# Performance work log

Hardware: AMD Instinct MI355X
Metric: run time of the kernel (lower is better)

The kernel has to match this reference:

```python
import jax, jax.numpy as jnp
import numpy as np
from math import sqrt

B, N, M, HID, NH = 16, 512, 1024, 512, 8
HS = HID // NH  # 64


def layer_norm(x, g, b, eps=1e-5):
    mu = jnp.mean(x, axis=-1, keepdims=True)
    var = jnp.var(x, axis=-1, keepdims=True)
    return (x - mu) * jax.lax.rsqrt(var + eps) * g + b


def apply_moverz(x, s, c):
    # x: [B, L, NH, HS]; s, c: [B, L, 1, HS//2]
    x0, x1 = x[..., 0::2], x[..., 1::2]
    return jnp.concatenate([x0 * c - x1 * s, x1 * c + x0 * s], axis=-1)


def attention(q, k, v, mask):
    # q: [B,Nq,NH,HS], k/v: [B,Nk,NH,HS], mask broadcastable to [B,NH,Nq,Nk]
    attn = jnp.einsum('bnhd,bmhd->bhnm', q, k) / sqrt(HS)
    attn = jnp.where(mask, -jnp.inf, attn)
    attn = jax.nn.softmax(attn, axis=-1)
    x = jnp.einsum('bhnm,bmhd->bnhd', attn, v)
    return x.reshape(x.shape[0], x.shape[1], HID)


def setup_inputs() -> dict:
    key = jax.random.key(0)
    ks = jax.random.split(key, 24)
    inp = {}
    inp['tgt'] = jax.random.normal(ks[0], (B, N, HID), dtype=jnp.float32)
    inp['mem'] = jax.random.normal(ks[1], (B, M, HID), dtype=jnp.float32)
    th_p = jax.random.uniform(ks[2], (B, N, 1, HS // 2), dtype=jnp.float32) * (2 * np.pi)
    th_k = jax.random.uniform(ks[3], (B, M, 1, HS // 2), dtype=jnp.float32) * (2 * np.pi)
    inp['pep_mass_sin'] = jnp.sin(th_p)
    inp['pep_mass_cos'] = jnp.cos(th_p)
    inp['peaks_moverz_sin'] = jnp.sin(th_k)
    inp['peaks_moverz_cos'] = jnp.cos(th_k)
    # causal self-attn mask (True = masked)
    inp['tgt_mask'] = jnp.triu(jnp.ones((N, N), dtype=bool), k=1)[None, None]
    # pad last 64 memory positions
    pad = jnp.arange(M) >= (M - 64)
    inp['mem_key_padding_mask'] = jnp.broadcast_to(pad[None, None, None, :], (B, 1, 1, M))
    s = 0.02
    w = lambda i, shape: jax.random.normal(ks[i], shape, dtype=jnp.float32) * s
    # MaskedMultiHeadAttn params
    inp['mmha_w'] = w(4, (3 * HID, HID)); inp['mmha_b'] = jnp.zeros((3 * HID,), jnp.float32)
    inp['mmha_ow'] = w(5, (HID, HID)); inp['mmha_ob'] = jnp.zeros((HID,), jnp.float32)
    inp['mmha_g'] = jnp.ones((HID,), jnp.float32); inp['mmha_beta'] = jnp.zeros((HID,), jnp.float32)
    # MultiHeadAttn (cross) params
    inp['mha_qw'] = w(6, (HID, HID)); inp['mha_qb'] = jnp.zeros((HID,), jnp.float32)
    inp['mha_kvw'] = w(7, (2 * HID, HID)); inp['mha_kvb'] = jnp.zeros((2 * HID,), jnp.float32)
    inp['mha_ow'] = w(8, (HID, HID)); inp['mha_ob'] = jnp.zeros((HID,), jnp.float32)
    inp['mha_g'] = jnp.ones((HID,), jnp.float32); inp['mha_beta'] = jnp.zeros((HID,), jnp.float32)
    # FFN params (no bias)
    inp['ffn_w1'] = w(9, (4 * HID, HID))
    inp['ffn_w2'] = w(10, (HID, 4 * HID))
    inp['ffn_g'] = jnp.ones((HID,), jnp.float32); inp['ffn_beta'] = jnp.zeros((HID,), jnp.float32)
    return inp


def reference(tgt, mem, pep_mass_sin, pep_mass_cos, peaks_moverz_sin, peaks_moverz_cos,
              tgt_mask, mem_key_padding_mask,
              mmha_w, mmha_b, mmha_ow, mmha_ob, mmha_g, mmha_beta,
              mha_qw, mha_qb, mha_kvw, mha_kvb, mha_ow, mha_ob, mha_g, mha_beta,
              ffn_w1, ffn_w2, ffn_g, ffn_beta):
    # --- masked self-attention ---
    qkv = (tgt @ mmha_w.T + mmha_b).reshape(B, N, NH, 3 * HS)
    q, k, v = jnp.split(qkv, 3, axis=-1)
    x = attention(q, k, v, tgt_mask)
    tgt = layer_norm(x @ mmha_ow.T + mmha_ob + tgt, mmha_g, mmha_beta)
    # --- cross-attention with moverz distance bias ---
    q = (tgt @ mha_qw.T + mha_qb).reshape(B, N, NH, HS)
    q = apply_moverz(q, pep_mass_sin, pep_mass_cos)
    kv = (mem @ mha_kvw.T + mha_kvb).reshape(B, M, NH, 2 * HS)
    k, v = jnp.split(kv, 2, axis=-1)
    k = apply_moverz(k, peaks_moverz_sin, peaks_moverz_cos)
    x = attention(q, k, v, mem_key_padding_mask)
    tgt = layer_norm(x @ mha_ow.T + mha_ob + tgt, mha_g, mha_beta)
    # --- FFN ---
    h = jax.nn.relu(tgt @ ffn_w1.T) @ ffn_w2.T
    tgt = layer_norm(tgt + h, ffn_g, ffn_beta)
    return tgt
```

## Files before the change

### kernel.cpp

```cpp
#include <hip/hip_runtime.h>
#include <hip/hip_bf16.h>

#define BB 16
#define NN 512
#define MM 1024
#define HIDD 512
#define NHH 8

typedef unsigned short ushort_t;
typedef __attribute__((ext_vector_type(8))) short short8;
typedef __attribute__((ext_vector_type(8))) _Float16 half8;
typedef __attribute__((ext_vector_type(4))) _Float16 half4;
typedef __attribute__((ext_vector_type(4))) float f32x4;

__device__ __forceinline__ ushort_t f2bf(float x) {
    unsigned u = __float_as_uint(x);
    u += 0x7fff + ((u >> 16) & 1);
    return (ushort_t)(u >> 16);
}

#define GLD16(g, l) __builtin_amdgcn_global_load_lds(                      \
    (const __attribute__((address_space(1))) void*)(g),                    \
    (__attribute__((address_space(3))) void*)(l), 16, 0, 0)

__device__ __forceinline__ void xcd_swizzle(int& colb, int& rowb) {
    int id = blockIdx.x + blockIdx.y * gridDim.x;
    int C = gridDim.x;
    int xcd = id & 7;
    int slot = id >> 3;
    int rows_per = gridDim.y >> 3;
    colb = slot % C;
    rowb = xcd * rows_per + slot / C;
}

__global__ __launch_bounds__(256)
void gemm_bf(const ushort_t* __restrict__ A, const ushort_t* __restrict__ W,
             const float* __restrict__ bias, float* __restrict__ C,
             ushort_t* __restrict__ Cb, _Float16* __restrict__ Ch,
             int K, int Cout, int relu) {
    __shared__ __align__(16) ushort_t smem[2][8192];
    const int tid = threadIdx.x;
    const int lane = tid & 63;
    const int wid = tid >> 6;
    const int wm = wid >> 1, wn = wid & 1;
    int colb, rowb;
    xcd_swizzle(colb, rowb);
    const long row0 = (long)rowb * 128;
    const long col0 = (long)colb * 128;

    const int sr = lane >> 2;
    const int skq = lane & 3;
    const ushort_t* Ag = A + (row0 + wid * 32 + sr) * (long)K + skq * 8;
    const ushort_t* Wg = W + (col0 + wid * 32 + sr) * (long)K + skq * 8;
    const int sa0 = (wid * 32) * 32, sa1 = (wid * 32 + 16) * 32;

    f32x4 acc[4][4] = {};
    const int lr = lane & 15;
    const int kg = lane >> 4;

    GLD16(Ag, &smem[0][sa0]);
    GLD16(Ag + 16 * (long)K, &smem[0][sa1]);
    GLD16(Wg, &smem[0][4096 + sa0]);
    GLD16(Wg + 16 * (long)K, &smem[0][4096 + sa1]);

    int pb = 0;
    for (int k0 = 0; k0 < K; k0 += 32, pb ^= 1) {
        __syncthreads();
        int kn = k0 + 32;
        if (kn < K) {
            GLD16(Ag + kn, &smem[pb ^ 1][sa0]);
            GLD16(Ag + 16 * (long)K + kn, &smem[pb ^ 1][sa1]);
            GLD16(Wg + kn, &smem[pb ^ 1][4096 + sa0]);
            GLD16(Wg + 16 * (long)K + kn, &smem[pb ^ 1][4096 + sa1]);
        }
        const ushort_t* Ab = smem[pb];
        const ushort_t* Wb = smem[pb] + 4096;
        short8 af[4], bfr[4];
#pragma unroll
        for (int i = 0; i < 4; i++)
            af[i] = *(const short8*)&Ab[(wm * 64 + i * 16 + lr) * 32 + kg * 8];
#pragma unroll
        for (int j = 0; j < 4; j++)
            bfr[j] = *(const short8*)&Wb[(wn * 64 + j * 16 + lr) * 32 + kg * 8];
#pragma unroll
        for (int i = 0; i < 4; i++)
#pragma unroll
            for (int j = 0; j < 4; j++)
                acc[i][j] = __builtin_amdgcn_mfma_f32_16x16x32_bf16(
                    af[i], bfr[j], acc[i][j], 0, 0, 0);
    }

#pragma unroll
    for (int i = 0; i < 4; i++) {
#pragma unroll
        for (int j = 0; j < 4; j++) {
            long row = row0 + wm * 64 + i * 16 + kg * 4;
            long col = col0 + wn * 64 + j * 16 + lr;
            float bv = bias ? bias[col] : 0.f;
#pragma unroll
            for (int r = 0; r < 4; r++) {
                float x = acc[i][j][r] + bv;
                if (relu) x = fmaxf(x, 0.f);
                size_t idx = (row + r) * (size_t)Cout + col;
                if (Ch)      Ch[idx] = (_Float16)x;
                else if (Cb) Cb[idx] = f2bf(x);
                else         C[idx] = x;
            }
        }
    }
}

__global__ __launch_bounds__(256)
void gemm_bf64(const ushort_t* __restrict__ A, const ushort_t* __restrict__ W,
               const float* __restrict__ bias, float* __restrict__ C,
               ushort_t* __restrict__ Cb, _Float16* __restrict__ Ch,
               int K, int Cout, int relu) {
    __shared__ __align__(16) ushort_t smem[2][6144];
    const int tid = threadIdx.x;
    const int lane = tid & 63;
    const int w = tid >> 6;
    int colb, rowb;
    xcd_swizzle(colb, rowb);
    const long row0 = (long)rowb * 128;
    const long col0 = (long)colb * 64;

    const int sr = lane >> 2;
    const int skq = lane & 3;
    const ushort_t* Ag = A + (row0 + w * 32 + sr) * (long)K + skq * 8;
    const ushort_t* Wg = W + (col0 + w * 16 + sr) * (long)K + skq * 8;
    const int sa0 = (w * 32) * 32, sa1 = (w * 32 + 16) * 32;
    const int sw0 = 4096 + (w * 16) * 32;

    f32x4 acc[2][4] = {};
    const int lr = lane & 15;
    const int kg = lane >> 4;

    GLD16(Ag, &smem[0][sa0]);
    GLD16(Ag + 16 * (long)K, &smem[0][sa1]);
    GLD16(Wg, &smem[0][sw0]);

    int pb = 0;
    for (int k0 = 0; k0 < K; k0 += 32, pb ^= 1) {
        __syncthreads();
        int kn = k0 + 32;
        if (kn < K) {
            GLD16(Ag + kn, &smem[pb ^ 1][sa0]);
            GLD16(Ag + 16 * (long)K + kn, &smem[pb ^ 1][sa1]);
            GLD16(Wg + kn, &smem[pb ^ 1][sw0]);
        }
        const ushort_t* Ab = smem[pb];
        const ushort_t* Wb = smem[pb] + 4096;
        short8 af[2], bfr[4];
#pragma unroll
        for (int i = 0; i < 2; i++)
            af[i] = *(const short8*)&Ab[(w * 32 + i * 16 + lr) * 32 + kg * 8];
#pragma unroll
        for (int j = 0; j < 4; j++)
            bfr[j] = *(const short8*)&Wb[(j * 16 + lr) * 32 + kg * 8];
#pragma unroll
        for (int i = 0; i < 2; i++)
#pragma unroll
            for (int j = 0; j < 4; j++)
                acc[i][j] = __builtin_amdgcn_mfma_f32_16x16x32_bf16(
                    af[i], bfr[j], acc[i][j], 0, 0, 0);
    }

#pragma unroll
    for (int i = 0; i < 2; i++) {
#pragma unroll
        for (int j = 0; j < 4; j++) {
            long row = row0 + w * 32 + i * 16 + kg * 4;
            long col = col0 + j * 16 + lr;
            float bv = bias ? bias[col] : 0.f;
#pragma unroll
            for (int r = 0; r < 4; r++) {
                float x = acc[i][j][r] + bv;
                if (relu) x = fmaxf(x, 0.f);
                size_t idx = (row + r) * (size_t)Cout + col;
                if (Ch)      Ch[idx] = (_Float16)x;
                else if (Cb) Cb[idx] = f2bf(x);
                else         C[idx] = x;
            }
        }
    }
}

__global__ __launch_bounds__(256)
void gemm_q_rot(const ushort_t* __restrict__ A, const ushort_t* __restrict__ W,
                const float* __restrict__ bias,
                const float* __restrict__ sn, const float* __restrict__ cs,
                _Float16* __restrict__ Qrot) {
    __shared__ __align__(16) ushort_t smem[2][6144];
    _Float16* Cs = (_Float16*)smem;
    const int K = 512;
    const int tid = threadIdx.x;
    const int lane = tid & 63;
    const int w = tid >> 6;
    int colb, rowb;
    xcd_swizzle(colb, rowb);
    const long row0 = (long)rowb * 128;
    const int h = colb;
    const long col0 = (long)h * 64;

    const int sr = lane >> 2;
    const int skq = lane & 3;
    const ushort_t* Ag = A + (row0 + w * 32 + sr) * (long)K + skq * 8;
    const ushort_t* Wg = W + (col0 + w * 16 + sr) * (long)K + skq * 8;
    const int sa0 = (w * 32) * 32, sa1 = (w * 32 + 16) * 32;
    const int sw0 = 4096 + (w * 16) * 32;

    f32x4 acc[2][4] = {};
    const int lr = lane & 15;
    const int kg = lane >> 4;

    GLD16(Ag, &smem[0][sa0]);
    GLD16(Ag + 16 * (long)K, &smem[0][sa1]);
    GLD16(Wg, &smem[0][sw0]);

    int pb = 0;
    for (int k0 = 0; k0 < K; k0 += 32, pb ^= 1) {
        __syncthreads();
        int kn = k0 + 32;
        if (kn < K) {
            GLD16(Ag + kn, &smem[pb ^ 1][sa0]);
            GLD16(Ag + 16 * (long)K + kn, &smem[pb ^ 1][sa1]);
            GLD16(Wg + kn, &smem[pb ^ 1][sw0]);
        }
        const ushort_t* Ab = smem[pb];
        const ushort_t* Wb = smem[pb] + 4096;
        short8 af[2], bfr[4];
#pragma unroll
        for (int i = 0; i < 2; i++)
            af[i] = *(const short8*)&Ab[(w * 32 + i * 16 + lr) * 32 + kg * 8];
#pragma unroll
        for (int j = 0; j < 4; j++)
            bfr[j] = *(const short8*)&Wb[(j * 16 + lr) * 32 + kg * 8];
#pragma unroll
        for (int i = 0; i < 2; i++)
#pragma unroll
            for (int j = 0; j < 4; j++)
                acc[i][j] = __builtin_amdgcn_mfma_f32_16x16x32_bf16(
                    af[i], bfr[j], acc[i][j], 0, 0, 0);
    }

    __syncthreads();
#pragma unroll
    for (int i = 0; i < 2; i++)
#pragma unroll
        for (int j = 0; j < 4; j++) {
            int row = w * 32 + i * 16 + kg * 4;
            int col = j * 16 + lr;
            float bv = bias[col0 + col];
#pragma unroll
            for (int r = 0; r < 4; r++)
                Cs[(row + r) * 76 + col] = (_Float16)(acc[i][j][r] + bv);
        }
    __syncthreads();
    for (int idx = tid; idx < 4096; idx += 256) {
        int rr = idx >> 5, j = idx & 31;
        size_t srow = (size_t)row0 + rr;
        float x0 = (float)Cs[rr * 76 + 2 * j], x1 = (float)Cs[rr * 76 + 2 * j + 1];
        float s = sn[srow * 32 + j], c = cs[srow * 32 + j];
        Qrot[srow * 512 + h * 64 + j]      = (_Float16)(x0 * c - x1 * s);
        Qrot[srow * 512 + h * 64 + 32 + j] = (_Float16)(x1 * c + x0 * s);
    }
}

__global__ __launch_bounds__(256)
void gemm_kv(const ushort_t* __restrict__ A, const ushort_t* __restrict__ W,
             const float* __restrict__ bias,
             const float* __restrict__ sn, const float* __restrict__ cs,
             _Float16* __restrict__ Krot, _Float16* __restrict__ Vth) {
    __shared__ __align__(16) ushort_t smem[2][8192];
    _Float16* Cs = (_Float16*)smem;
    const int K = 512;
    const int tid = threadIdx.x;
    const int lane = tid & 63;
    const int wid = tid >> 6;
    const int wm = wid >> 1, wn = wid & 1;
    int colb, rowb;
    xcd_swizzle(colb, rowb);
    const long row0 = (long)rowb * 128;
    const int h = colb;
    const long col0 = (long)h * 128;

    const int sr = lane >> 2;
    const int skq = lane & 3;
    const ushort_t* Ag = A + (row0 + wid * 32 + sr) * (long)K + skq * 8;
    const ushort_t* Wg = W + (col0 + wid * 32 + sr) * (long)K + skq * 8;
    const int sa0 = (wid * 32) * 32, sa1 = (wid * 32 + 16) * 32;

    f32x4 acc[4][4] = {};
    const int lr = lane & 15;
    const int kg = lane >> 4;

    GLD16(Ag, &smem[0][sa0]);
    GLD16(Ag + 16 * (long)K, &smem[0][sa1]);
    GLD16(Wg, &smem[0][4096 + sa0]);
    GLD16(Wg + 16 * (long)K, &smem[0][4096 + sa1]);

    int pb = 0;
    for (int k0 = 0; k0 < K; k0 += 32, pb ^= 1) {
        __syncthreads();
        int kn = k0 + 32;
        if (kn < K) {
            GLD16(Ag + kn, &smem[pb ^ 1][sa0]);
            GLD16(Ag + 16 * (long)K + kn, &smem[pb ^ 1][sa1]);
            GLD16(Wg + kn, &smem[pb ^ 1][4096 + sa0]);
            GLD16(Wg + 16 * (long)K + kn, &smem[pb ^ 1][4096 + sa1]);
        }
        const ushort_t* Ab = smem[pb];
        const ushort_t* Wb = smem[pb] + 4096;
        short8 af[4], bfr[4];
#pragma unroll
        for (int i = 0; i < 4; i++)
            af[i] = *(const short8*)&Ab[(wm * 64 + i * 16 + lr) * 32 + kg * 8];
#pragma unroll
        for (int j = 0; j < 4; j++)
            bfr[j] = *(const short8*)&Wb[(wn * 64 + j * 16 + lr) * 32 + kg * 8];
#pragma unroll
        for (int i = 0; i < 4; i++)
#pragma unroll
            for (int j = 0; j < 4; j++)
                acc[i][j] = __builtin_amdgcn_mfma_f32_16x16x32_bf16(
                    af[i], bfr[j], acc[i][j], 0, 0, 0);
    }

    const int b_ = (int)(row0 >> 10);
    const int m0_ = (int)(row0 & 1023);
#pragma unroll
    for (int half = 0; half < 2; half++) {
        __syncthreads();
        if (wn == half) {
#pragma unroll
            for (int i = 0; i < 4; i++)
#pragma unroll
                for (int j = 0; j < 4; j++) {
                    int row = wm * 64 + i * 16 + kg * 4;
                    int col = j * 16 + lr;
                    float bv = bias[col0 + half * 64 + col];
#pragma unroll
                    for (int r = 0; r < 4; r++)
                        Cs[(row + r) * 76 + col] = (_Float16)(acc[i][j][r] + bv);
                }
        }
        __syncthreads();
        if (half == 0) {
            for (int idx = tid; idx < 4096; idx += 256) {
                int rr = idx >> 5, j = idx & 31;
                size_t srow = (size_t)row0 + rr;
                float x0 = (float)Cs[rr * 76 + 2 * j], x1 = (float)Cs[rr * 76 + 2 * j + 1];
                float s = sn[srow * 32 + j], c = cs[srow * 32 + j];
                Krot[srow * 512 + h * 64 + j]      = (_Float16)(x0 * c - x1 * s);
                Krot[srow * 512 + h * 64 + 32 + j] = (_Float16)(x1 * c + x0 * s);
            }
        } else {
            for (int idx = tid; idx < 1024; idx += 256) {
                int d = idx >> 4, c = idx & 15;
                half8 v;
#pragma unroll
                for (int k = 0; k < 8; k++) v[k] = Cs[(c * 8 + k) * 76 + d];
                *(half8*)(Vth + (((size_t)(b_ * NHH + h)) * 64 + d) * MM
                          + m0_ + c * 8) = v;
            }
        }
    }
}

__global__ __launch_bounds__(256)
void cvt_all(const float* __restrict__ tgt, const float* __restrict__ mem,
             const float* __restrict__ w0, const float* __restrict__ w1,
             const float* __restrict__ w2, const float* __restrict__ w3,
             const float* __restrict__ w4, const float* __restrict__ w5,
             const float* __restrict__ w6,
             ushort_t* __restrict__ Abf, ushort_t* __restrict__ membf,
             ushort_t* __restrict__ Wbf) {
    int blk = blockIdx.x;
    const float* src;
    ushort_t* dst;
    size_t off;
    if (blk < 4096)       { src = tgt; dst = Abf;   off = (size_t)blk * 1024; }
    else if (blk < 12288) { src = mem; dst = membf; off = (size_t)(blk - 4096) * 1024; }
    else {
        int wb = blk - 12288;
        dst = Wbf + (size_t)wb * 1024;
        if (wb < 768)       { src = w0; off = (size_t)wb * 1024; }
        else if (wb < 1024) { src = w1; off = (size_t)(wb - 768) * 1024; }
        else if (wb < 1280) { src = w2; off = (size_t)(wb - 1024) * 1024; }
        else if (wb < 1792) { src = w3; off = (size_t)(wb - 1280) * 1024; }
        else if (wb < 2048) { src = w4; off = (size_t)(wb - 1792) * 1024; }
        else if (wb < 3072) { src = w5; off = (size_t)(wb - 2048) * 1024; }
        else                { src = w6; off = (size_t)(wb - 3072) * 1024; }
        float4 v = *(const float4*)(src + off + threadIdx.x * 4);
        ushort4 o;
        o.x = f2bf(v.x); o.y = f2bf(v.y); o.z = f2bf(v.z); o.w = f2bf(v.w);
        *(ushort4*)(dst + threadIdx.x * 4) = o;
        return;
    }
    float4 v = *(const float4*)(src + off + threadIdx.x * 4);
    ushort4 o;
    o.x = f2bf(v.x); o.y = f2bf(v.y); o.z = f2bf(v.z); o.w = f2bf(v.w);
    *(ushort4*)(dst + off + threadIdx.x * 4) = o;
}

__global__ __launch_bounds__(256)
void prep_vt(const _Float16* __restrict__ src, int L, int stride,
             int hmul, int hadd, _Float16* __restrict__ Vt) {
    const int b = blockIdx.z, h = blockIdx.y, m0 = blockIdx.x * 64;
    const int tid = threadIdx.x;
    __shared__ _Float16 vt[64][72];
    for (int idx = tid; idx < 512; idx += 256) {
        int m = idx >> 3, c = idx & 7;
        half8 v = *(const half8*)(src + ((size_t)(b * L + m0 + m)) * stride
                                  + h * hmul + hadd + c * 8);
#pragma unroll
        for (int k = 0; k < 8; k++) vt[c * 8 + k][m] = v[k];
    }
    __syncthreads();
    for (int idx = tid; idx < 512; idx += 256) {
        int d = idx >> 3, c = idx & 7;
        *(half8*)(Vt + (((size_t)(b * NHH + h)) * 64 + d) * L + m0 + c * 8)
            = *(const half8*)&vt[d][c * 8];
    }
}

__global__ __launch_bounds__(256)
void attn2(const _Float16* __restrict__ Q, int qstride, int qmul, int qadd,
           const _Float16* __restrict__ K, int kstride, int kmul, int kadd,
           const _Float16* __restrict__ Vt, int LV, int Lrows,
           ushort_t* __restrict__ out, int kvlen, int causal) {
    const int g = blockIdx.x;
    const int bh = (g & 7) * 16 + ((g >> 3) & 15);
    const int qb = g >> 7;
    const int b = bh >> 3, h = bh & 7;
    const int n0 = qb * 128;
    const int tid = threadIdx.x, lane = tid & 63, w = tid >> 6;
    const int quad = lane >> 4, l16 = lane & 15;
    const int qw = n0 + w * 32;

    __shared__ _Float16 Ks[64 * 72];
    __shared__ _Float16 Vs[64 * 72];
    __shared__ _Float16 Ps[4][32 * 72];
    _Float16* Pw = Ps[w];

    half8 bq[2][2];
#pragma unroll
    for (int s = 0; s < 2; s++)
#pragma unroll
        for (int c = 0; c < 2; c++)
            bq[s][c] = *(const half8*)(Q + ((size_t)(b * NN + qw + s * 16 + l16)) * qstride
                                       + h * qmul + qadd + c * 32 + quad * 8);

    f32x4 acc[2][4] = {};
    float mrun[2] = {-3e38f, -3e38f}, lrun[2] = {0.f, 0.f};

    const int srow = tid >> 3;
    const int scol = (tid & 7) * 8;
    const int limit = causal ? (n0 + 128) : kvlen;

    half8 kr0, kr1, vr0, vr1;
    {
        size_t kb = ((size_t)(b * Lrows + srow)) * kstride + h * kmul + kadd + scol;
        kr0 = *(const half8*)(K + kb);
        kr1 = *(const half8*)(K + kb + (size_t)32 * kstride);
        size_t vb = (((size_t)(b * NHH + h)) * 64 + srow) * (size_t)LV + scol;
        vr0 = *(const half8*)(Vt + vb);
        vr1 = *(const half8*)(Vt + vb + (size_t)32 * LV);
    }

    for (int key0 = 0; key0 < limit; key0 += 64) {
        __syncthreads();
        *(half8*)&Ks[srow * 72 + scol] = kr0;
        *(half8*)&Ks[(srow + 32) * 72 + scol] = kr1;
        *(half8*)&Vs[srow * 72 + scol] = vr0;
        *(half8*)&Vs[(srow + 32) * 72 + scol] = vr1;
        __syncthreads();
        int knext = key0 + 64;
        if (knext < limit) {
            size_t kb = ((size_t)(b * Lrows + knext + srow)) * kstride
                        + h * kmul + kadd + scol;
            kr0 = *(const half8*)(K + kb);
            kr1 = *(const half8*)(K + kb + (size_t)32 * kstride);
            size_t vb = (((size_t)(b * NHH + h)) * 64 + srow) * (size_t)LV
                        + knext + scol;
            vr0 = *(const half8*)(Vt + vb);
            vr1 = *(const half8*)(Vt + vb + (size_t)32 * LV);
        }
        if (causal && key0 > qw + 31) continue;

        f32x4 st[2][4];
#pragma unroll
        for (int kt = 0; kt < 4; kt++) {
            half8 ak0 = *(const half8*)&Ks[(kt * 16 + l16) * 72 + quad * 8];
            half8 ak1 = *(const half8*)&Ks[(kt * 16 + l16) * 72 + 32 + quad * 8];
#pragma unroll
            for (int s = 0; s < 2; s++) {
                f32x4 z = {};
                z = __builtin_amdgcn_mfma_f32_16x16x32_f16(ak0, bq[s][0], z, 0, 0, 0);
                z = __builtin_amdgcn_mfma_f32_16x16x32_f16(ak1, bq[s][1], z, 0, 0, 0);
                st[s][kt] = z;
            }
        }
        if (causal && key0 + 64 > qw) {
#pragma unroll
            for (int s = 0; s < 2; s++) {
                int qabs = qw + s * 16 + l16;
#pragma unroll
                for (int kt = 0; kt < 4; kt++)
#pragma unroll
                    for (int r = 0; r < 4; r++)
                        if (key0 + kt * 16 + quad * 4 + r > qabs)
                            st[s][kt][r] = -3e38f;
            }
        }
#pragma unroll
        for (int s = 0; s < 2; s++) {
            float lm = -3e38f;
#pragma unroll
            for (int kt = 0; kt < 4; kt++)
                lm = fmaxf(lm, fmaxf(fmaxf(st[s][kt][0], st[s][kt][1]),
                                     fmaxf(st[s][kt][2], st[s][kt][3])));
            lm = fmaxf(lm, __shfl_xor(lm, 16));
            lm = fmaxf(lm, __shfl_xor(lm, 32));
            float mnew = fmaxf(mrun[s], lm);
            float corr = __expf((mrun[s] - mnew) * 0.125f);
            mrun[s] = mnew;
            float ls = 0.f;
#pragma unroll
            for (int kt = 0; kt < 4; kt++) {
                half4 ph;
#pragma unroll
                for (int r = 0; r < 4; r++) {
                    float p = __expf((st[s][kt][r] - mnew) * 0.125f);
                    ls += p;
                    ph[r] = (_Float16)p;
                }
                *(half4*)&Pw[(s * 16 + l16) * 72 + kt * 16 + quad * 4] = ph;
            }
            ls += __shfl_xor(ls, 16);
            ls += __shfl_xor(ls, 32);
            lrun[s] = lrun[s] * corr + ls;
            float cb0 = __shfl(corr, (lane & 48) | (quad * 4 + 0));
            float cb1 = __shfl(corr, (lane & 48) | (quad * 4 + 1));
            float cb2 = __shfl(corr, (lane & 48) | (quad * 4 + 2));
            float cb3 = __shfl(corr, (lane & 48) | (quad * 4 + 3));
#pragma unroll
            for (int dt = 0; dt < 4; dt++) {
                acc[s][dt][0] *= cb0; acc[s][dt][1] *= cb1;
                acc[s][dt][2] *= cb2; acc[s][dt][3] *= cb3;
            }
        }
        half8 ap[2][2];
#pragma unroll
        for (int s = 0; s < 2; s++)
#pragma unroll
            for (int c = 0; c < 2; c++)
                ap[s][c] = *(const half8*)&Pw[(s * 16 + l16) * 72 + c * 32 + quad * 8];
#pragma unroll
        for (int dt = 0; dt < 4; dt++) {
            half8 bv0 = *(const half8*)&Vs[(dt * 16 + l16) * 72 + quad * 8];
            half8 bv1 = *(const half8*)&Vs[(dt * 16 + l16) * 72 + 32 + quad * 8];
#pragma unroll
            for (int s = 0; s < 2; s++) {
                acc[s][dt] = __builtin_amdgcn_mfma_f32_16x16x32_f16(ap[s][0], bv0, acc[s][dt], 0, 0, 0);
                acc[s][dt] = __builtin_amdgcn_mfma_f32_16x16x32_f16(ap[s][1], bv1, acc[s][dt], 0, 0, 0);
            }
        }
    }
#pragma unroll
    for (int s = 0; s < 2; s++) {
        float invq = 1.f / lrun[s];
        float iv0 = __shfl(invq, (lane & 48) | (quad * 4 + 0));
        float iv1 = __shfl(invq, (lane & 48) | (quad * 4 + 1));
        float iv2 = __shfl(invq, (lane & 48) | (quad * 4 + 2));
        float iv3 = __shfl(invq, (lane & 48) | (quad * 4 + 3));
#pragma unroll
        for (int dt = 0; dt < 4; dt++) {
            size_t base = ((size_t)(b * NN + qw + s * 16 + quad * 4)) * 512
                          + h * 64 + dt * 16 + l16;
            out[base]           = f2bf(acc[s][dt][0] * iv0);
            out[base + 512]     = f2bf(acc[s][dt][1] * iv1);
            out[base + 1024]    = f2bf(acc[s][dt][2] * iv2);
            out[base + 1536]    = f2bf(acc[s][dt][3] * iv3);
        }
    }
}

__global__ __launch_bounds__(256)
void ln_residual(const float* __restrict__ u, int nsplit,
                 const float* __restrict__ res,
                 const float* __restrict__ g, const float* __restrict__ be,
                 float* __restrict__ out, ushort_t* __restrict__ outbf) {
    const int row = blockIdx.x, t = threadIdx.x;
    const float* rp = res + (size_t)row * HIDD;
    float z0 = rp[t];
    float z1 = rp[t + 256];
    for (int s = 0; s < nsplit; s++) {
        const float* up = u + (size_t)s * 4194304 + (size_t)row * HIDD;
        z0 += up[t];
        z1 += up[t + 256];
    }
    float sm = z0 + z1, s2 = z0 * z0 + z1 * z1;
#pragma unroll
    for (int off = 1; off < 64; off <<= 1) {
        sm += __shfl_xor(sm, off, 64);
        s2 += __shfl_xor(s2, off, 64);
    }
    __shared__ float ps[4], ps2[4];
    int w = t >> 6;
    if ((t & 63) == 0) { ps[w] = sm; ps2[w] = s2; }
    __syncthreads();
    sm = ps[0] + ps[1] + ps[2] + ps[3];
    s2 = ps2[0] + ps2[1] + ps2[2] + ps2[3];
    float mu = sm * (1.f / 512.f);
    float var = s2 * (1.f / 512.f) - mu * mu;
    float rstd = rsqrtf(var + 1e-5f);
    float y0 = (z0 - mu) * rstd * g[t] + be[t];
    float y1 = (z1 - mu) * rstd * g[t + 256] + be[t + 256];
    out[(size_t)row * HIDD + t]       = y0;
    out[(size_t)row * HIDD + t + 256] = y1;
    if (outbf) {
        outbf[(size_t)row * HIDD + t]       = f2bf(y0);
        outbf[(size_t)row * HIDD + t + 256] = f2bf(y1);
    }
}

extern "C" void kernel_launch(void* const* d_in, const int* in_sizes, int n_in,
                              void* d_out, int out_size, void* d_ws, size_t ws_size,
                              hipStream_t stream) {
    const float* tgt      = (const float*)d_in[0];
    const float* mem      = (const float*)d_in[1];
    const float* pep_sin  = (const float*)d_in[2];
    const float* pep_cos  = (const float*)d_in[3];
    const float* pk_sin   = (const float*)d_in[4];
    const float* pk_cos   = (const float*)d_in[5];
    const float* mmha_w   = (const float*)d_in[8];
    const float* mmha_b   = (const float*)d_in[9];
    const float* mmha_ow  = (const float*)d_in[10];
    const float* mmha_ob  = (const float*)d_in[11];
    const float* mmha_g   = (const float*)d_in[12];
    const float* mmha_be  = (const float*)d_in[13];
    const float* mha_qw   = (const float*)d_in[14];
    const float* mha_qb   = (const float*)d_in[15];
    const float* mha_kvw  = (const float*)d_in[16];
    const float* mha_kvb  = (const float*)d_in[17];
    const float* mha_ow   = (const float*)d_in[18];
    const float* mha_ob   = (const float*)d_in[19];
    const float* mha_g    = (const float*)d_in[20];
    const float* mha_be   = (const float*)d_in[21];
    const float* ffn_w1   = (const float*)d_in[22];
    const float* ffn_w2   = (const float*)d_in[23];
    const float* ffn_g    = (const float*)d_in[24];
    const float* ffn_be   = (const float*)d_in[25];

    float* ws = (float*)d_ws;
    float* utmp  = ws;
    float* tgt12 = ws + 4194304;
    _Float16* hp = (_Float16*)(ws + 8388608);
    _Float16* qkvh  = hp;
    _Float16* Qrot  = hp + 12582912;
    _Float16* Vth   = hp + 16777216;
    _Float16* Krot  = hp + 25165824;
    ushort_t* membf = (ushort_t*)(hp + 33554432);
    ushort_t* Abf   = (ushort_t*)(hp + 41943040);
    ushort_t* Wbf   = (ushort_t*)(hp + 46137344);
    ushort_t* w_mmha = Wbf;
    ushort_t* w_mmow = Wbf + 786432;
    ushort_t* w_qw   = Wbf + 1048576;
    ushort_t* w_kvw  = Wbf + 1310720;
    ushort_t* w_mow  = Wbf + 1835008;
    ushort_t* w_f1   = Wbf + 2097152;
    ushort_t* w_f2   = Wbf + 3145728;
    ushort_t* hbf = (ushort_t*)qkvh;
    float* out = (float*)d_out;
    (void)in_sizes; (void)n_in; (void)out_size; (void)ws_size;

    cvt_all<<<16384, 256, 0, stream>>>(tgt, mem, mmha_w, mmha_ow, mha_qw,
                                       mha_kvw, mha_ow, ffn_w1, ffn_w2,
                                       Abf, membf, Wbf);
    gemm_bf<<<dim3(12, 64), 256, 0, stream>>>(Abf, w_mmha, mmha_b, nullptr, nullptr, qkvh, 512, 1536, 0);
    prep_vt<<<dim3(8, NHH, BB), 256, 0, stream>>>(qkvh, NN, 1536, 192, 128, Vth);
    attn2<<<512, 256, 0, stream>>>(qkvh, 1536, 192, 0, qkvh, 1536, 192, 64,
                                   Vth, NN, NN, Abf, 0, 1);
    gemm_bf64<<<dim3(8, 64), 256, 0, stream>>>(Abf, w_mmow, mmha_ob, utmp, nullptr, nullptr, 512, 512, 0);
    ln_residual<<<8192, 256, 0, stream>>>(utmp, 1, tgt, mmha_g, mmha_be, tgt12, Abf);
    gemm_q_rot<<<dim3(8, 64), 256, 0, stream>>>(Abf, w_qw, mha_qb, pep_sin, pep_cos, Qrot);
    gemm_kv<<<dim3(8, 128), 256, 0, stream>>>(membf, w_kvw, mha_kvb, pk_sin, pk_cos, Krot, Vth);
    attn2<<<512, 256, 0, stream>>>(Qrot, 512, 64, 0, Krot, 512, 64, 0,
                                   Vth, MM, MM, Abf, MM - 64, 0);
    gemm_bf64<<<dim3(8, 64), 256, 0, stream>>>(Abf, w_mow, mha_ob, utmp, nullptr, nullptr, 512, 512, 0);
    ln_residual<<<8192, 256, 0, stream>>>(utmp, 1, tgt12, mha_g, mha_be, tgt12, Abf);
    gemm_bf<<<dim3(16, 64), 256, 0, stream>>>(Abf, w_f1, nullptr, nullptr, hbf, nullptr, 512, 2048, 1);
    gemm_bf64<<<dim3(8, 64), 256, 0, stream>>>(hbf, w_f2, nullptr, utmp, nullptr, nullptr, 2048, 512, 0);
    ln_residual<<<8192, 256, 0, stream>>>(utmp, 1, tgt12, ffn_g, ffn_be, out, nullptr);
}
```

Measured before the change: 414.5 us.

## Halve attention query tile to 64 rows and double grid size

Result: no change. 422.3 us (+1.9%).

```diff
diff --git a/kernel.cpp b/kernel.cpp
--- a/kernel.cpp
+++ b/kernel.cpp
@@ -425,7 +425,7 @@
 }
 
 __global__ __launch_bounds__(256)
-void attn2(const _Float16* __restrict__ Q, int qstride, int qmul, int qadd,
+void attn3(const _Float16* __restrict__ Q, int qstride, int qmul, int qadd,
            const _Float16* __restrict__ K, int kstride, int kmul, int kadd,
            const _Float16* __restrict__ Vt, int LV, int Lrows,
            ushort_t* __restrict__ out, int kvlen, int causal) {
@@ -433,30 +433,29 @@
     const int bh = (g & 7) * 16 + ((g >> 3) & 15);
     const int qb = g >> 7;
     const int b = bh >> 3, h = bh & 7;
-    const int n0 = qb * 128;
+    const int n0 = qb * 64;
     const int tid = threadIdx.x, lane = tid & 63, w = tid >> 6;
     const int quad = lane >> 4, l16 = lane & 15;
-    const int qw = n0 + w * 32;
-
-    __shared__ _Float16 Ks[64 * 72];
-    __shared__ _Float16 Vs[64 * 72];
-    __shared__ _Float16 Ps[4][32 * 72];
+    const int qw = n0 + w * 16;
+    const float SC = 0.125f * 1.44269504089f;
+
+    __shared__ _Float16 Ks[64 * 76];
+    __shared__ _Float16 Vs[64 * 76];
+    __shared__ _Float16 Ps[4][16 * 76];
     _Float16* Pw = Ps[w];
 
-    half8 bq[2][2];
-#pragma unroll
-    for (int s = 0; s < 2; s++)
-#pragma unroll
-        for (int c = 0; c < 2; c++)
-            bq[s][c] = *(const half8*)(Q + ((size_t)(b * NN + qw + s * 16 + l16)) * qstride
-                                       + h * qmul + qadd + c * 32 + quad * 8);
-
-    f32x4 acc[2][4] = {};
-    float mrun[2] = {-3e38f, -3e38f}, lrun[2] = {0.f, 0.f};
+    half8 bq[2];
+#pragma unroll
+    for (int c = 0; c < 2; c++)
+        bq[c] = *(const half8*)(Q + ((size_t)(b * NN + qw + l16)) * qstride
+                                + h * qmul + qadd + c * 32 + quad * 8);
+
+    f32x4 acc[4] = {};
+    float mrun = -3e38f, lrun = 0.f;
 
     const int srow = tid >> 3;
     const int scol = (tid & 7) * 8;
-    const int limit = causal ? (n0 + 128) : kvlen;
+    const int limit = causal ? (n0 + 64) : kvlen;
 
     half8 kr0, kr1, vr0, vr1;
     {
@@ -470,10 +469,10 @@
 
     for (int key0 = 0; key0 < limit; key0 += 64) {
         __syncthreads();
-        *(half8*)&Ks[srow * 72 + scol] = kr0;
-        *(half8*)&Ks[(srow + 32) * 72 + scol] = kr1;
-        *(half8*)&Vs[srow * 72 + scol] = vr0;
-        *(half8*)&Vs[(srow + 32) * 72 + scol] = vr1;
+        *(half8*)&Ks[srow * 76 + scol] = kr0;
+        *(half8*)&Ks[(srow + 32) * 76 + scol] = kr1;
+        *(half8*)&Vs[srow * 76 + scol] = vr0;
+        *(half8*)&Vs[(srow + 32) * 76 + scol] = vr1;
         __syncthreads();
         int knext = key0 + 64;
         if (knext < limit) {
@@ -486,103 +485,84 @@
             vr0 = *(const half8*)(Vt + vb);
             vr1 = *(const half8*)(Vt + vb + (size_t)32 * LV);
         }
-        if (causal && key0 > qw + 31) continue;
-
-        f32x4 st[2][4];
+        if (causal && key0 > qw + 15) continue;
+
+        f32x4 st[4];
 #pragma unroll
         for (int kt = 0; kt < 4; kt++) {
-            half8 ak0 = *(const half8*)&Ks[(kt * 16 + l16) * 72 + quad * 8];
-            half8 ak1 = *(const half8*)&Ks[(kt * 16 + l16) * 72 + 32 + quad * 8];
-#pragma unroll
-            for (int s = 0; s < 2; s++) {
-                f32x4 z = {};
-                z = __builtin_amdgcn_mfma_f32_16x16x32_f16(ak0, bq[s][0], z, 0, 0, 0);
-                z = __builtin_amdgcn_mfma_f32_16x16x32_f16(ak1, bq[s][1], z, 0, 0, 0);
-                st[s][kt] = z;
+            half8 ak0 = *(const half8*)&Ks[(kt * 16 + l16) * 76 + quad * 8];
+            half8 ak1 = *(const half8*)&Ks[(kt * 16 + l16) * 76 + 32 + quad * 8];
+            f32x4 z = {};
+            z = __builtin_amdgcn_mfma_f32_16x16x32_f16(ak0, bq[0], z, 0, 0, 0);
+            z = __builtin_amdgcn_mfma_f32_16x16x32_f16(ak1, bq[1], z, 0, 0, 0);
+            st[kt] = z;
+        }
+        if (causal && key0 + 63 > qw) {
+            int qabs = qw + l16;
+#pragma unroll
+            for (int kt = 0; kt < 4; kt++)
+#pragma unroll
+                for (int r = 0; r < 4; r++)
+                    if (key0 + kt * 16 + quad * 4 + r > qabs)
+                        st[kt][r] = -3e38f;
+        }
+        float lm = -3e38f;
+#pragma unroll
+        for (int kt = 0; kt < 4; kt++)
+            lm = fmaxf(lm, fmaxf(fmaxf(st[kt][0], st[kt][1]),
+                                 fmaxf(st[kt][2], st[kt][3])));
+        lm = fmaxf(lm, __shfl_xor(lm, 16));
+        lm = fmaxf(lm, __shfl_xor(lm, 32));
+        float mnew = fmaxf(mrun, lm);
+        float corr = exp2f((mrun - mnew) * SC);
+        mrun = mnew;
+        float ls = 0.f;
+#pragma unroll
+        for (int kt = 0; kt < 4; kt++) {
+            half4 ph;
+#pragma unroll
+            for (int r = 0; r < 4; r++) {
+                float p = exp2f((st[kt][r] - mnew) * SC);
+                ls += p;
+                ph[r] = (_Float16)p;
             }
-        }
-        if (causal && key0 + 64 > qw) {
-#pragma unroll
-            for (int s = 0; s < 2; s++) {
-                int qabs = qw + s * 16 + l16;
-#pragma unroll
-                for (int kt = 0; kt < 4; kt++)
-#pragma unroll
-                    for (int r = 0; r < 4; r++)
-                        if (key0 + kt * 16 + quad * 4 + r > qabs)
-                            st[s][kt][r] = -3e38f;
-            }
-        }
-#pragma unroll
-        for (int s = 0; s < 2; s++) {
-            float lm = -3e38f;
-#pragma unroll
-            for (int kt = 0; kt < 4; kt++)
-                lm = fmaxf(lm, fmaxf(fmaxf(st[s][kt][0], st[s][kt][1]),
-                                     fmaxf(st[s][kt][2], st[s][kt][3])));
-            lm = fmaxf(lm, __shfl_xor(lm, 16));
-            lm = fmaxf(lm, __shfl_xor(lm, 32));
-            float mnew = fmaxf(mrun[s], lm);
-            float corr = __expf((mrun[s] - mnew) * 0.125f);
-            mrun[s] = mnew;
-            float ls = 0.f;
-#pragma unroll
-            for (int kt = 0; kt < 4; kt++) {
-                half4 ph;
-#pragma unroll
-                for (int r = 0; r < 4; r++) {
-                    float p = __expf((st[s][kt][r] - mnew) * 0.125f);
-                    ls += p;
-                    ph[r] = (_Float16)p;
-                }
-                *(half4*)&Pw[(s * 16 + l16) * 72 + kt * 16 + quad * 4] = ph;
-            }
-            ls += __shfl_xor(ls, 16);
-            ls += __shfl_xor(ls, 32);
-            lrun[s] = lrun[s] * corr + ls;
-            float cb0 = __shfl(corr, (lane & 48) | (quad * 4 + 0));
-            float cb1 = __shfl(corr, (lane & 48) | (quad * 4 + 1));
-            float cb2 = __shfl(corr, (lane & 48) | (quad * 4 + 2));
-            float cb3 = __shfl(corr, (lane & 48) | (quad * 4 + 3));
-#pragma unroll
-            for (int dt = 0; dt < 4; dt++) {
-                acc[s][dt][0] *= cb0; acc[s][dt][1] *= cb1;
-                acc[s][dt][2] *= cb2; acc[s][dt][3] *= cb3;
-            }
-        }
-        half8 ap[2][2];
-#pragma unroll
-        for (int s = 0; s < 2; s++)
-#pragma unroll
-            for (int c = 0; c < 2; c++)
-                ap[s][c] = *(const half8*)&Pw[(s * 16 + l16) * 72 + c * 32 + quad * 8];
+            *(half4*)&Pw[l16 * 76 + kt * 16 + quad * 4] = ph;
+        }
+        ls += __shfl_xor(ls, 16);
+        ls += __shfl_xor(ls, 32);
+        lrun = lrun * corr + ls;
+        float cb0 = __shfl(corr, (lane & 48) | (quad * 4 + 0));
+        float cb1 = __shfl(corr, (lane & 48) | (quad * 4 + 1));
+        float cb2 = __shfl(corr, (lane & 48) | (quad * 4 + 2));
+        float cb3 = __shfl(corr, (lane & 48) | (quad * 4 + 3));
 #pragma unroll
         for (int dt = 0; dt < 4; dt++) {
-            half8 bv0 = *(const half8*)&Vs[(dt * 16 + l16) * 72 + quad * 8];
-            half8 bv1 = *(const half8*)&Vs[(dt * 16 + l16) * 72 + 32 + quad * 8];
-#pragma unroll
-            for (int s = 0; s < 2; s++) {
-                acc[s][dt] = __builtin_amdgcn_mfma_f32_16x16x32_f16(ap[s][0], bv0, acc[s][dt], 0, 0, 0);
-                acc[s][dt] = __builtin_amdgcn_mfma_f32_16x16x32_f16(ap[s][1], bv1, acc[s][dt], 0, 0, 0);
-            }
-        }
-    }
-#pragma unroll
-    for (int s = 0; s < 2; s++) {
-        float invq = 1.f / lrun[s];
-        float iv0 = __shfl(invq, (lane & 48) | (quad * 4 + 0));
-        float iv1 = __shfl(invq, (lane & 48) | (quad * 4 + 1));
-        float iv2 = __shfl(invq, (lane & 48) | (quad * 4 + 2));
-        float iv3 = __shfl(invq, (lane & 48) | (quad * 4 + 3));
+            acc[dt][0] *= cb0; acc[dt][1] *= cb1;
+            acc[dt][2] *= cb2; acc[dt][3] *= cb3;
+        }
+        half8 ap0 = *(const half8*)&Pw[l16 * 76 + quad * 8];
+        half8 ap1 = *(const half8*)&Pw[l16 * 76 + 32 + quad * 8];
 #pragma unroll
         for (int dt = 0; dt < 4; dt++) {
-            size_t base = ((size_t)(b * NN + qw + s * 16 + quad * 4)) * 512
-                          + h * 64 + dt * 16 + l16;
-            out[base]           = f2bf(acc[s][dt][0] * iv0);
-            out[base + 512]     = f2bf(acc[s][dt][1] * iv1);
-            out[base + 1024]    = f2bf(acc[s][dt][2] * iv2);
-            out[base + 1536]    = f2bf(acc[s][dt][3] * iv3);
-        }
+            half8 bv0 = *(const half8*)&Vs[(dt * 16 + l16) * 76 + quad * 8];
+            half8 bv1 = *(const half8*)&Vs[(dt * 16 + l16) * 76 + 32 + quad * 8];
+            acc[dt] = __builtin_amdgcn_mfma_f32_16x16x32_f16(ap0, bv0, acc[dt], 0, 0, 0);
+            acc[dt] = __builtin_amdgcn_mfma_f32_16x16x32_f16(ap1, bv1, acc[dt], 0, 0, 0);
+        }
+    }
+    float invq = 1.f / lrun;
+    float iv0 = __shfl(invq, (lane & 48) | (quad * 4 + 0));
+    float iv1 = __shfl(invq, (lane & 48) | (quad * 4 + 1));
+    float iv2 = __shfl(invq, (lane & 48) | (quad * 4 + 2));
+    float iv3 = __shfl(invq, (lane & 48) | (quad * 4 + 3));
+#pragma unroll
+    for (int dt = 0; dt < 4; dt++) {
+        size_t base = ((size_t)(b * NN + qw + quad * 4)) * 512
+                      + h * 64 + dt * 16 + l16;
+        out[base]        = f2bf(acc[dt][0] * iv0);
+        out[base + 512]  = f2bf(acc[dt][1] * iv1);
+        out[base + 1024] = f2bf(acc[dt][2] * iv2);
+        out[base + 1536] = f2bf(acc[dt][3] * iv3);
     }
 }
 
@@ -680,14 +660,14 @@
                                        Abf, membf, Wbf);
     gemm_bf<<<dim3(12, 64), 256, 0, stream>>>(Abf, w_mmha, mmha_b, nullptr, nullptr, qkvh, 512, 1536, 0);
     prep_vt<<<dim3(8, NHH, BB), 256, 0, stream>>>(qkvh, NN, 1536, 192, 128, Vth);
-    attn2<<<512, 256, 0, stream>>>(qkvh, 1536, 192, 0, qkvh, 1536, 192, 64,
-                                   Vth, NN, NN, Abf, 0, 1);
+    attn3<<<1024, 256, 0, stream>>>(qkvh, 1536, 192, 0, qkvh, 1536, 192, 64,
+                                    Vth, NN, NN, Abf, 0, 1);
     gemm_bf64<<<dim3(8, 64), 256, 0, stream>>>(Abf, w_mmow, mmha_ob, utmp, nullptr, nullptr, 512, 512, 0);
     ln_residual<<<8192, 256, 0, stream>>>(utmp, 1, tgt, mmha_g, mmha_be, tgt12, Abf);
     gemm_q_rot<<<dim3(8, 64), 256, 0, stream>>>(Abf, w_qw, mha_qb, pep_sin, pep_cos, Qrot);
     gemm_kv<<<dim3(8, 128), 256, 0, stream>>>(membf, w_kvw, mha_kvb, pk_sin, pk_cos, Krot, Vth);
-    attn2<<<512, 256, 0, stream>>>(Qrot, 512, 64, 0, Krot, 512, 64, 0,
-                                   Vth, MM, MM, Abf, MM - 64, 0);
+    attn3<<<1024, 256, 0, stream>>>(Qrot, 512, 64, 0, Krot, 512, 64, 0,
+                                    Vth, MM, MM, Abf, MM - 64, 0);
     gemm_bf64<<<dim3(8, 64), 256, 0, stream>>>(Abf, w_mow, mha_ob, utmp, nullptr, nullptr, 512, 512, 0);
     ln_residual<<<8192, 256, 0, stream>>>(utmp, 1, tgt12, mha_g, mha_be, tgt12, Abf);
     gemm_bf<<<dim3(16, 64), 256, 0, stream>>>(Abf, w_f1, nullptr, nullptr, hbf, nullptr, 512, 2048, 1);
```
